# Kernel tuning notes

Measured on AMD Instinct MI355X. Metric: run time of the kernel, lower is better.

## Reference

```python
import jax, jax.numpy as jnp
import numpy as np

B, TQ, TK, D, F, H = 16, 256, 256, 256, 36, 8
DK = D // H          # dk = d // h
SF = int(np.sqrt(F)) # 6
MASK_VALUE = -1e30


def setup_inputs() -> dict:
    rng = jax.random.key(0)
    ks = jax.random.split(rng, 12)
    s = 0.05
    return {
        "query": jax.random.normal(ks[0], (B, TQ, D), jnp.float32),
        "key_ts": jax.random.normal(ks[1], (B, TK, D), jnp.float32),
        "value": jax.random.normal(ks[2], (B, TK, F), jnp.float32),
        "mask": (jax.random.uniform(ks[3], (B, TK, F)) < 0.5).astype(jnp.float32),
        "Wq": jax.random.normal(ks[4], (H, D, DK), jnp.float32) * s,
        "Wk": jax.random.normal(ks[5], (H, D, DK), jnp.float32) * s,
        "Wc": jax.random.normal(ks[6], (H, D), jnp.float32) * s,
        "bc": jnp.zeros((D,), jnp.float32),
        "Wo_1": jax.random.normal(ks[7], (F, SF), jnp.float32) * s,
        "bo_1": jnp.zeros((SF,), jnp.float32),
        "Wo_2": jax.random.normal(ks[8], (SF, 1), jnp.float32) * s,
        "bo_2": jnp.zeros((D,), jnp.float32),
    }


def reference(query, key_ts, value, mask, Wq, Wk, Wc, bc, Wo_1, bo_1, Wo_2, bo_2):
    # mask: [B, Tk, F] 0/1 missingness indicator -> broadcast as [B, 1, Tk, F]
    m = mask[:, None, :, :]
    heads = []
    for j in range(Wq.shape[0]):  # fixed small head loop (h=8)
        q = query @ Wq[j]                                  # [B, Tq, dk]
        k = key_ts @ Wk[j]                                 # [B, Tk, dk]
        A = jnp.einsum('bqd,bkd->bqk', q, k)[..., None]    # [B, Tq, Tk, 1] (no 1/sqrt(dk) scaling, as in original)
        A = m * A + (1.0 - m) * MASK_VALUE                 # [B, Tq, Tk, F]
        A = jax.nn.softmax(A, axis=-2)                     # softmax over Tk, per feature
        heads.append(jnp.einsum('bqkf,bkf->bqf', A, value))  # masked weighted sum
    latent = jnp.stack(heads, axis=-1)                     # [B, Tq, F, h]
    # permute (0,2,1,3) -> [B, F, Tq, h]; dot Wc[h,d] -> [B, F, Tq, d]
    latent = jnp.tanh(jnp.einsum('bqfh,hd->bfqd', latent, Wc) + bc)
    # permute (0,2,3,1) -> [B, Tq, d, F]; Wo_1: F -> sqrt(F)
    x = jnp.tanh(jnp.einsum('bfqd,fs->bqds', latent, Wo_1) + bo_1)
    # Wo_2: sqrt(F) -> 1, squeeze, add bo_2 -> [B, Tq, d]
    x = jnp.einsum('bqds,so->bqd', x, Wo_2) + bo_2
    return x
```

## Files before the change

kernel.cpp:

```cpp
#include <hip/hip_runtime.h>

#define NB 16
#define NTQ 256
#define NTK 256
#define ND 256
#define NF 36
#define NH 8
#define NDK 32
#define NSF 6

typedef __attribute__((ext_vector_type(8))) short short8;
typedef __attribute__((ext_vector_type(4))) float f32x4;
#define MFMA16(a,b,c) __builtin_amdgcn_mfma_f32_16x16x32_bf16(a,b,c,0,0,0)

#define SZ_X   (16*256*256*2)
#define XQH_OFF 0
#define XQL_OFF (XQH_OFF + SZ_X)
#define XKH_OFF (XQL_OFF + SZ_X)
#define XKL_OFF (XKH_OFF + SZ_X)
#define SZ_WT  (2*256*256*2)
#define WTH_OFF (XKL_OFF + SZ_X)
#define WTL_OFF (WTH_OFF + SZ_WT)
#define SZ_QP  (16*8*256*32*2)
#define QPH_OFF (WTL_OFF + SZ_WT)
#define QPL_OFF (QPH_OFF + SZ_QP)
#define KPH_OFF (QPL_OFF + SZ_QP)
#define KPL_OFF (KPH_OFF + SZ_QP)
#define SZ_RT  (16*80*256*2)
#define RT_OFF  (KPL_OFF + SZ_QP)
#define HD_OFF  (RT_OFF + SZ_RT)

__device__ __forceinline__ short f2bf(float x){
    union { float f; unsigned u; } v; v.f = x;
    unsigned r = v.u + 0x7fffu + ((v.u >> 16) & 1u);
    return (short)(r >> 16);
}
__device__ __forceinline__ float bf2f(short s){
    union { float f; unsigned u; } v; v.u = ((unsigned)(unsigned short)s) << 16;
    return v.f;
}
__device__ __forceinline__ float fast_tanh(float x){
    float e = __expf(2.0f*x);
    return 1.0f - 2.0f/(e + 1.0f);
}
__device__ __forceinline__ short8 ld8(const short* p){ return *(const short8*)p; }

__global__ void imta_pack_x(const float* __restrict__ query, const float* __restrict__ key_ts,
                            char* __restrict__ wsb){
    int i = blockIdx.x*256 + threadIdx.x;
    short* qh = (short*)(wsb + XQH_OFF); short* ql = (short*)(wsb + XQL_OFF);
    short* kh = (short*)(wsb + XKH_OFF); short* kl = (short*)(wsb + XKL_OFF);
    float q = query[i];
    short h = f2bf(q); qh[i] = h; ql[i] = f2bf(q - bf2f(h));
    float k = key_ts[i];
    short h2 = f2bf(k); kh[i] = h2; kl[i] = f2bf(k - bf2f(h2));
}

__global__ void imta_pack_w(const float* __restrict__ Wq, const float* __restrict__ Wk,
                            char* __restrict__ wsb){
    int idx = blockIdx.x*256 + threadIdx.x;
    int side = idx >> 16, rem = idx & 65535;
    int n = rem >> 8, d = rem & 255;
    int j = n >> 5, dk = n & 31;
    float w = (side ? Wk : Wq)[(j*ND + d)*NDK + dk];
    short* wh = (short*)(wsb + WTH_OFF) + side*65536;
    short* wl = (short*)(wsb + WTL_OFF) + side*65536;
    short h = f2bf(w);
    wh[n*256 + d] = h; wl[n*256 + d] = f2bf(w - bf2f(h));
}

__global__ void imta_pack_rt(const float* __restrict__ mask, const float* __restrict__ value,
                             char* __restrict__ wsb){
    int f = blockIdx.x, b = blockIdx.y, k = threadIdx.x;
    short* rt = (short*)(wsb + RT_OFF) + b*80*256;
    if (f < NF){
        float m = mask [(b*NTK + k)*NF + f];
        float v = value[(b*NTK + k)*NF + f];
        rt[(2*f    )*256 + k] = f2bf(m*v);
        rt[(2*f + 1)*256 + k] = f2bf(m);
    } else {
        rt[(2*f    )*256 + k] = 0;
        rt[(2*f + 1)*256 + k] = 0;
    }
}

__global__ void imta_proj(char* __restrict__ wsb){
    const int mt = blockIdx.x >> 1, nh = blockIdx.x & 1;
    const int side = blockIdx.y, b = blockIdx.z;
    const int tid = threadIdx.x, w = tid >> 6, lane = tid & 63;
    const int col = lane & 15, quad = lane >> 4;
    const int t0 = mt*64;
    const short* XH = (const short*)(wsb + (side ? XKH_OFF : XQH_OFF)) + b*NTQ*ND;
    const short* XL = (const short*)(wsb + (side ? XKL_OFF : XQL_OFF)) + b*NTQ*ND;
    const short* WH = (const short*)(wsb + WTH_OFF) + side*65536;
    const short* WL = (const short*)(wsb + WTL_OFF) + side*65536;
    f32x4 acc[4][2];
    #pragma unroll
    for (int m = 0; m < 4; ++m){ acc[m][0] = (f32x4)0.f; acc[m][1] = (f32x4)0.f; }
    for (int kb = 0; kb < 8; ++kb){
        const int ko = kb*32 + quad*8;
        short8 ah[4], al[4], bh[2], bl[2];
        #pragma unroll
        for (int m = 0; m < 4; ++m){
            const int t = t0 + m*16 + col;
            ah[m] = ld8(XH + t*ND + ko);
            al[m] = ld8(XL + t*ND + ko);
        }
        #pragma unroll
        for (int nt = 0; nt < 2; ++nt){
            const int n = (nh*8 + w*2 + nt)*16 + col;
            bh[nt] = ld8(WH + n*256 + ko);
            bl[nt] = ld8(WL + n*256 + ko);
        }
        #pragma unroll
        for (int m = 0; m < 4; ++m)
            #pragma unroll
            for (int nt = 0; nt < 2; ++nt){
                acc[m][nt] = MFMA16(al[m], bh[nt], acc[m][nt]);
                acc[m][nt] = MFMA16(ah[m], bl[nt], acc[m][nt]);
                acc[m][nt] = MFMA16(ah[m], bh[nt], acc[m][nt]);
            }
    }
    short* oh = (short*)(wsb + (side ? KPH_OFF : QPH_OFF));
    short* ol = (short*)(wsb + (side ? KPL_OFF : QPL_OFF));
    #pragma unroll
    for (int m = 0; m < 4; ++m)
        #pragma unroll
        for (int nt = 0; nt < 2; ++nt){
            const int n = (nh*8 + w*2 + nt)*16 + col;
            const int j = n >> 5, dk = n & 31;
            #pragma unroll
            for (int r = 0; r < 4; ++r){
                const int t = t0 + m*16 + quad*4 + r;
                float v = acc[m][nt][r];
                short h = f2bf(v);
                size_t o = (size_t)(((b*NH + j)*NTQ + t)*NDK + dk);
                oh[o] = h; ol[o] = f2bf(v - bf2f(h));
            }
        }
}

__global__ void imta_attn(char* __restrict__ wsb, const float* __restrict__ value){
    const int t0 = blockIdx.x*64;
    const int j = blockIdx.y, b = blockIdx.z;
    const int tid = threadIdx.x, w = tid >> 6, lane = tid & 63;
    const int col = lane & 15, quad = lane >> 4;
    __shared__ short sE[64*264];
    const short* QH = (const short*)(wsb + QPH_OFF) + (b*NH + j)*NTQ*NDK;
    const short* QL = (const short*)(wsb + QPL_OFF) + (b*NH + j)*NTQ*NDK;
    const short* KH = (const short*)(wsb + KPH_OFF) + (b*NH + j)*NTK*NDK;
    const short* KL = (const short*)(wsb + KPL_OFF) + (b*NH + j)*NTK*NDK;
    const short* RT = (const short*)(wsb + RT_OFF) + b*80*256;
    float* HD = (float*)(wsb + HD_OFF) + (b*NH + j)*NTQ*NF;

    short8 ah[4], al[4];
    #pragma unroll
    for (int m = 0; m < 4; ++m){
        const int t = t0 + m*16 + col;
        ah[m] = ld8(QH + t*NDK + quad*8);
        al[m] = ld8(QL + t*NDK + quad*8);
    }
    #pragma unroll
    for (int nt = 0; nt < 4; ++nt){
        const int key0 = w*64 + nt*16;
        short8 bh = ld8(KH + (key0 + col)*NDK + quad*8);
        short8 bl = ld8(KL + (key0 + col)*NDK + quad*8);
        f32x4 acc[4];
        #pragma unroll
        for (int m = 0; m < 4; ++m){
            f32x4 c = (f32x4)0.f;
            c = MFMA16(al[m], bh, c);
            c = MFMA16(ah[m], bl, c);
            c = MFMA16(ah[m], bh, c);
            acc[m] = c;
        }
        const int key = key0 + col;
        #pragma unroll
        for (int m = 0; m < 4; ++m)
            #pragma unroll
            for (int r = 0; r < 4; ++r){
                const int q = m*16 + quad*4 + r;
                sE[q*264 + key] = f2bf(__expf(acc[m][r]));
            }
    }
    __syncthreads();

    const int q0 = w*16;
    f32x4 acc2[5];
    #pragma unroll
    for (int nt = 0; nt < 5; ++nt) acc2[nt] = (f32x4)0.f;
    #pragma unroll 2
    for (int kb = 0; kb < 8; ++kb){
        const int ko = kb*32 + quad*8;
        short8 a = *(const short8*)&sE[(q0 + col)*264 + ko];
        #pragma unroll
        for (int nt = 0; nt < 5; ++nt){
            short8 bb = ld8(RT + (nt*16 + col)*256 + ko);
            acc2[nt] = MFMA16(a, bb, acc2[nt]);
        }
    }
    __syncthreads();
    float* sH = (float*)sE;
    #pragma unroll
    for (int nt = 0; nt < 5; ++nt)
        #pragma unroll
        for (int r = 0; r < 4; ++r){
            float v = acc2[nt][r];
            float o = __shfl_xor(v, 1, 64);
            if (!(col & 1)){
                const int f = nt*8 + (col >> 1);
                if (f < NF){
                    float num = v, den = o, h;
                    if (den != 0.0f) h = num/den;
                    else {
                        float s = 0.f;
                        for (int k = 0; k < NTK; ++k) s += value[(b*NTK + k)*NF + f];
                        h = s * (1.0f/256.0f);
                    }
                    sH[(q0 + quad*4 + r)*40 + f] = h;
                }
            }
        }
    __syncthreads();
    for (int idx = tid; idx < 64*NF; idx += 256){
        const int q = idx/NF, f = idx - q*NF;
        HD[(t0 + q)*NF + f] = sH[q*40 + f];
    }
}

__global__ void imta_final(const float* __restrict__ Wc, const float* __restrict__ bc,
                           const float* __restrict__ Wo1, const float* __restrict__ bo1,
                           const float* __restrict__ Wo2, const float* __restrict__ bo2,
                           const float* __restrict__ hd, float* __restrict__ out){
    const int bq = blockIdx.x;
    const int b = bq >> 8, qq = bq & 255;
    const int tid = threadIdx.x;
    __shared__ float sh[NF*NH];
    __shared__ float sW1[NF*NSF];
    for (int t = tid; t < NF*NH; t += 256){
        int jj = t/NF, f = t - jj*NF;
        sh[t] = hd[((b*NH + jj)*NTQ + qq)*NF + f];
    }
    if (tid < NF*NSF) sW1[tid] = Wo1[tid];
    __syncthreads();
    const int d = tid;
    float wcr[8];
    #pragma unroll
    for (int h = 0; h < 8; ++h) wcr[h] = Wc[h*ND + d];
    const float bcd = bc[d];
    float a2[6];
    #pragma unroll
    for (int s = 0; s < 6; ++s) a2[s] = bo1[s];
    #pragma unroll
    for (int f4 = 0; f4 < NF; f4 += 4){
        float4 sv[8];
        #pragma unroll
        for (int h = 0; h < 8; ++h) sv[h] = *(const float4*)&sh[h*NF + f4];
        #pragma unroll
        for (int fi = 0; fi < 4; ++fi){
            float a = bcd;
            #pragma unroll
            for (int h = 0; h < 8; ++h)
                a = fmaf(reinterpret_cast<const float*>(&sv[h])[fi], wcr[h], a);
            float lf = fast_tanh(a);
            const int f = f4 + fi;
            #pragma unroll
            for (int s = 0; s < 6; ++s)
                a2[s] = fmaf(lf, sW1[f*NSF + s], a2[s]);
        }
    }
    float o = bo2[d];
    #pragma unroll
    for (int s = 0; s < 6; ++s)
        o = fmaf(fast_tanh(a2[s]), Wo2[s], o);
    out[(b*NTQ + qq)*ND + d] = o;
}

extern "C" void kernel_launch(void* const* d_in, const int* in_sizes, int n_in,
                              void* d_out, int out_size, void* d_ws, size_t ws_size,
                              hipStream_t stream){
    const float* query  = (const float*)d_in[0];
    const float* key_ts = (const float*)d_in[1];
    const float* value  = (const float*)d_in[2];
    const float* mask   = (const float*)d_in[3];
    const float* Wq     = (const float*)d_in[4];
    const float* Wk     = (const float*)d_in[5];
    const float* Wc     = (const float*)d_in[6];
    const float* bc     = (const float*)d_in[7];
    const float* Wo1    = (const float*)d_in[8];
    const float* bo1    = (const float*)d_in[9];
    const float* Wo2    = (const float*)d_in[10];
    const float* bo2    = (const float*)d_in[11];
    char* wsb  = (char*)d_ws;
    float* out = (float*)d_out;
    (void)in_sizes; (void)n_in; (void)out_size; (void)ws_size;

    imta_pack_x <<<dim3(4096),     dim3(256), 0, stream>>>(query, key_ts, wsb);
    imta_pack_w <<<dim3(512),      dim3(256), 0, stream>>>(Wq, Wk, wsb);
    imta_pack_rt<<<dim3(40, 16),   dim3(256), 0, stream>>>(mask, value, wsb);
    imta_proj   <<<dim3(8, 2, 16), dim3(256), 0, stream>>>(wsb);
    imta_attn   <<<dim3(4, 8, 16), dim3(256), 0, stream>>>(wsb, value);
    imta_final  <<<dim3(4096),     dim3(256), 0, stream>>>(Wc, bc, Wo1, bo1, Wo2, bo2,
                                                           (const float*)(wsb + HD_OFF), out);
}
```

Measured before the change: 154.8 us.

## Fuse bf16 split packing and mask/value packing into projection kernel

Removes the separate pack kernels for inputs, weights and mask/value. The projection now reads fp32 query/key and weights straight from global memory, stages them in shared memory, and converts them to hi/lo bf16 on the fly before the MFMAs. Mask/value packing runs as an extra grid slice of the same launch. This drops three launches and the round trip of the packed intermediates through global memory, at the cost of repeated conversions, a transposed shared-memory store for W, and smaller 32-row tiles per block.

```diff
diff --git a/kernel.cpp b/kernel.cpp
--- a/kernel.cpp
+++ b/kernel.cpp
@@ -13,16 +13,8 @@
 typedef __attribute__((ext_vector_type(4))) float f32x4;
 #define MFMA16(a,b,c) __builtin_amdgcn_mfma_f32_16x16x32_bf16(a,b,c,0,0,0)
 
-#define SZ_X   (16*256*256*2)
-#define XQH_OFF 0
-#define XQL_OFF (XQH_OFF + SZ_X)
-#define XKH_OFF (XQL_OFF + SZ_X)
-#define XKL_OFF (XKH_OFF + SZ_X)
-#define SZ_WT  (2*256*256*2)
-#define WTH_OFF (XKL_OFF + SZ_X)
-#define WTL_OFF (WTH_OFF + SZ_WT)
 #define SZ_QP  (16*8*256*32*2)
-#define QPH_OFF (WTL_OFF + SZ_WT)
+#define QPH_OFF 0
 #define QPL_OFF (QPH_OFF + SZ_QP)
 #define KPH_OFF (QPL_OFF + SZ_QP)
 #define KPL_OFF (KPH_OFF + SZ_QP)
@@ -45,75 +37,74 @@
 }
 __device__ __forceinline__ short8 ld8(const short* p){ return *(const short8*)p; }
 
-__global__ void imta_pack_x(const float* __restrict__ query, const float* __restrict__ key_ts,
-                            char* __restrict__ wsb){
-    int i = blockIdx.x*256 + threadIdx.x;
-    short* qh = (short*)(wsb + XQH_OFF); short* ql = (short*)(wsb + XQL_OFF);
-    short* kh = (short*)(wsb + XKH_OFF); short* kl = (short*)(wsb + XKL_OFF);
-    float q = query[i];
-    short h = f2bf(q); qh[i] = h; ql[i] = f2bf(q - bf2f(h));
-    float k = key_ts[i];
-    short h2 = f2bf(k); kh[i] = h2; kl[i] = f2bf(k - bf2f(h2));
-}
-
-__global__ void imta_pack_w(const float* __restrict__ Wq, const float* __restrict__ Wk,
-                            char* __restrict__ wsb){
-    int idx = blockIdx.x*256 + threadIdx.x;
-    int side = idx >> 16, rem = idx & 65535;
-    int n = rem >> 8, d = rem & 255;
-    int j = n >> 5, dk = n & 31;
-    float w = (side ? Wk : Wq)[(j*ND + d)*NDK + dk];
-    short* wh = (short*)(wsb + WTH_OFF) + side*65536;
-    short* wl = (short*)(wsb + WTL_OFF) + side*65536;
-    short h = f2bf(w);
-    wh[n*256 + d] = h; wl[n*256 + d] = f2bf(w - bf2f(h));
-}
-
-__global__ void imta_pack_rt(const float* __restrict__ mask, const float* __restrict__ value,
-                             char* __restrict__ wsb){
-    int f = blockIdx.x, b = blockIdx.y, k = threadIdx.x;
-    short* rt = (short*)(wsb + RT_OFF) + b*80*256;
-    if (f < NF){
-        float m = mask [(b*NTK + k)*NF + f];
-        float v = value[(b*NTK + k)*NF + f];
-        rt[(2*f    )*256 + k] = f2bf(m*v);
-        rt[(2*f + 1)*256 + k] = f2bf(m);
-    } else {
-        rt[(2*f    )*256 + k] = 0;
-        rt[(2*f + 1)*256 + k] = 0;
-    }
-}
-
-__global__ void imta_proj(char* __restrict__ wsb){
+__device__ __forceinline__ void cvt8(const float* __restrict__ p, short8& h8, short8& l8){
+    f32x4 a = *(const f32x4*)p;
+    f32x4 c = *(const f32x4*)(p + 4);
+    #pragma unroll
+    for (int i = 0; i < 4; ++i){
+        short h0 = f2bf(a[i]); h8[i]   = h0; l8[i]   = f2bf(a[i] - bf2f(h0));
+        short h1 = f2bf(c[i]); h8[4+i] = h1; l8[4+i] = f2bf(c[i] - bf2f(h1));
+    }
+}
+
+__global__ void imta_prep(const float* __restrict__ query, const float* __restrict__ key_ts,
+                          const float* __restrict__ Wq, const float* __restrict__ Wk,
+                          const float* __restrict__ mask, const float* __restrict__ value,
+                          char* __restrict__ wsb){
+    if (blockIdx.y == 2){
+        const int b = blockIdx.z, k = threadIdx.x;
+        short* rt = (short*)(wsb + RT_OFF) + b*80*256;
+        #pragma unroll
+        for (int r = 0; r < 5; ++r){
+            const int fp = blockIdx.x*5 + r;
+            const int f = fp >> 1;
+            short o = 0;
+            if (f < NF){
+                float m = mask[(b*NTK + k)*NF + f];
+                o = (fp & 1) ? f2bf(m) : f2bf(m * value[(b*NTK + k)*NF + f]);
+            }
+            rt[fp*256 + k] = o;
+        }
+        return;
+    }
+    const int side = blockIdx.y, b = blockIdx.z;
     const int mt = blockIdx.x >> 1, nh = blockIdx.x & 1;
-    const int side = blockIdx.y, b = blockIdx.z;
+    const int t0 = mt*32;
     const int tid = threadIdx.x, w = tid >> 6, lane = tid & 63;
     const int col = lane & 15, quad = lane >> 4;
-    const int t0 = mt*64;
-    const short* XH = (const short*)(wsb + (side ? XKH_OFF : XQH_OFF)) + b*NTQ*ND;
-    const short* XL = (const short*)(wsb + (side ? XKL_OFF : XQL_OFF)) + b*NTQ*ND;
-    const short* WH = (const short*)(wsb + WTH_OFF) + side*65536;
-    const short* WL = (const short*)(wsb + WTL_OFF) + side*65536;
-    f32x4 acc[4][2];
-    #pragma unroll
-    for (int m = 0; m < 4; ++m){ acc[m][0] = (f32x4)0.f; acc[m][1] = (f32x4)0.f; }
+    const float* __restrict__ X = side ? key_ts : query;
+    const float* __restrict__ W = side ? Wk : Wq;
+    __shared__ float sX[32][36];
+    __shared__ float sW[128][36];
+    const int xr = tid >> 3, xc = (tid & 7)*4;
+    const int dr = tid >> 3, dkq = (tid & 7)*4;
+    f32x4 acc[2][2];
+    #pragma unroll
+    for (int m = 0; m < 2; ++m){ acc[m][0] = (f32x4)0.f; acc[m][1] = (f32x4)0.f; }
     for (int kb = 0; kb < 8; ++kb){
-        const int ko = kb*32 + quad*8;
-        short8 ah[4], al[4], bh[2], bl[2];
-        #pragma unroll
-        for (int m = 0; m < 4; ++m){
-            const int t = t0 + m*16 + col;
-            ah[m] = ld8(XH + t*ND + ko);
-            al[m] = ld8(XL + t*ND + ko);
-        }
-        #pragma unroll
-        for (int nt = 0; nt < 2; ++nt){
-            const int n = (nh*8 + w*2 + nt)*16 + col;
-            bh[nt] = ld8(WH + n*256 + ko);
-            bl[nt] = ld8(WL + n*256 + ko);
-        }
-        #pragma unroll
-        for (int m = 0; m < 4; ++m)
+        const int dc = kb*32;
+        float4 xv = *(const float4*)(X + (size_t)(b*NTQ + t0 + xr)*ND + dc + xc);
+        float4 wv[4];
+        #pragma unroll
+        for (int jj = 0; jj < 4; ++jj)
+            wv[jj] = *(const float4*)(W + (size_t)((4*nh + jj)*ND + dc + dr)*NDK + dkq);
+        __syncthreads();
+        *(float4*)&sX[xr][xc] = xv;
+        #pragma unroll
+        for (int jj = 0; jj < 4; ++jj)
+            #pragma unroll
+            for (int i = 0; i < 4; ++i)
+                sW[jj*32 + dkq + i][dr] = ((const float*)&wv[jj])[i];
+        __syncthreads();
+        short8 ah[2], al[2], bh[2], bl[2];
+        #pragma unroll
+        for (int m = 0; m < 2; ++m)
+            cvt8(&sX[m*16 + col][quad*8], ah[m], al[m]);
+        #pragma unroll
+        for (int nt = 0; nt < 2; ++nt)
+            cvt8(&sW[(w*2 + nt)*16 + col][quad*8], bh[nt], bl[nt]);
+        #pragma unroll
+        for (int m = 0; m < 2; ++m)
             #pragma unroll
             for (int nt = 0; nt < 2; ++nt){
                 acc[m][nt] = MFMA16(al[m], bh[nt], acc[m][nt]);
@@ -124,7 +115,7 @@
     short* oh = (short*)(wsb + (side ? KPH_OFF : QPH_OFF));
     short* ol = (short*)(wsb + (side ? KPL_OFF : QPL_OFF));
     #pragma unroll
-    for (int m = 0; m < 4; ++m)
+    for (int m = 0; m < 2; ++m)
         #pragma unroll
         for (int nt = 0; nt < 2; ++nt){
             const int n = (nh*8 + w*2 + nt)*16 + col;
@@ -295,11 +286,8 @@
     float* out = (float*)d_out;
     (void)in_sizes; (void)n_in; (void)out_size; (void)ws_size;
 
-    imta_pack_x <<<dim3(4096),     dim3(256), 0, stream>>>(query, key_ts, wsb);
-    imta_pack_w <<<dim3(512),      dim3(256), 0, stream>>>(Wq, Wk, wsb);
-    imta_pack_rt<<<dim3(40, 16),   dim3(256), 0, stream>>>(mask, value, wsb);
-    imta_proj   <<<dim3(8, 2, 16), dim3(256), 0, stream>>>(wsb);
-    imta_attn   <<<dim3(4, 8, 16), dim3(256), 0, stream>>>(wsb, value);
-    imta_final  <<<dim3(4096),     dim3(256), 0, stream>>>(Wc, bc, Wo1, bo1, Wo2, bo2,
-                                                           (const float*)(wsb + HD_OFF), out);
-}
+    imta_prep <<<dim3(16, 3, 16), dim3(256), 0, stream>>>(query, key_ts, Wq, Wk, mask, value, wsb);
+    imta_attn <<<dim3(4, 8, 16),  dim3(256), 0, stream>>>(wsb, value);
+    imta_final<<<dim3(4096),      dim3(256), 0, stream>>>(Wc, bc, Wo1, bo1, Wo2, bo2,
+                                                          (const float*)(wsb + HD_OFF), out);
+}
```

Result: faster. 142.4 us (-8.0%).
